# Optimization experiments

Hardware: AMD Instinct MI355X
Metric: run time of the kernel (lower is better)

The kernel has to match this reference:

```python
import jax, jax.numpy as jnp
import numpy as np
from jax import lax

B, C, H, W = 2, 64, 384, 384
WS = 8; NH = 4; HD = C // NH; S = WS * WS  # 64 tokens per window
EPS = 1e-5


def setup_inputs() -> dict:
    key = jax.random.key(0)
    ks = jax.random.split(key, 16)
    def n(k, shape, s=0.02):
        return jax.random.normal(k, shape, jnp.float32) * s
    return {
        "x": jax.random.normal(ks[0], (B, C, H, W), jnp.float32),
        "norm1_w": jnp.ones((C,), jnp.float32), "norm1_b": jnp.zeros((C,), jnp.float32),
        "qkv_w": n(ks[1], (3 * C, C)), "qkv_b": jnp.zeros((3 * C,), jnp.float32),
        "pos_bias": n(ks[2], (1, S, NH, NH), 0.01),  # faithful: bias over (tokens, heads, heads)
        "out_w": n(ks[3], (C, C)), "out_b": jnp.zeros((C,), jnp.float32),
        "convp_w": n(ks[4], (C, C)), "convp_b": jnp.zeros((C,), jnp.float32),
        "pw1_w": n(ks[5], (C, C, 1)), "pw1_b": jnp.zeros((C,), jnp.float32),
        "dw1_w": n(ks[6], (C, 1, 3)), "dw1_b": jnp.zeros((C,), jnp.float32),
        "tok_w": n(ks[7], (C, C)), "tok_b": jnp.zeros((C,), jnp.float32),
        "norm2_w": jnp.ones((C,), jnp.float32), "norm2_b": jnp.zeros((C,), jnp.float32),
        "leff_pw_w": n(ks[8], (C, C, 1, 1)),
        "leff_dw_w": n(ks[9], (C, 1, 3, 3)), "leff_dw_b": jnp.zeros((C,), jnp.float32),
        "fc1_w": n(ks[10], (4 * C, C)), "fc1_b": jnp.zeros((4 * C,), jnp.float32),
        "fc2_w": n(ks[11], (C, 4 * C)), "fc2_b": jnp.zeros((C,), jnp.float32),
    }


def _ln_c(x, w, b):
    # channel-wise LayerNorm (Restormer 'WithBias') on (B,C,H,W), biased variance
    mu = x.mean(axis=1, keepdims=True)
    var = ((x - mu) ** 2).mean(axis=1, keepdims=True)
    return (x - mu) / jnp.sqrt(var + EPS) * w[None, :, None, None] + b[None, :, None, None]


def _lin(x, w, b):
    return x @ w.T + b


def _win_part(x):
    # (B,C,H,W) -> (B*nw, S, C); H,W divisible by WS so pad is a no-op
    b = x.shape[0]
    x = x.reshape(b, C, H // WS, WS, W // WS, WS)
    return x.transpose(0, 2, 4, 3, 5, 1).reshape(-1, S, C)


def _win_merge(wins):
    b = wins.shape[0] // ((H // WS) * (W // WS))
    x = wins.reshape(b, H // WS, W // WS, WS, WS, C)
    return x.transpose(0, 5, 1, 3, 2, 4).reshape(b, C, H, W)


def _remsa(xw, qkv_w, qkv_b, pos_bias, out_w, out_b, convp_w, convp_b,
           pw1_w, pw1_b, dw1_w, dw1_b, tok_w, tok_b):
    bw = xw.shape[0]
    qkv = _lin(xw, qkv_w, qkv_b).reshape(bw, S, NH, 3 * HD)
    q, k, v = jnp.split(qkv, 3, axis=-1)  # each (bw, S, NH, HD)
    # Faithful to source: NO head transpose -> attention mixes across the heads axis
    scores = jnp.einsum('bshd,bsgd->bshg', q, k) * (HD ** -0.5) + pos_bias  # (bw,S,NH,NH)
    attn = jax.nn.softmax(scores, axis=-1)
    ao = jnp.einsum('bshg,bsgd->bshd', attn, v).reshape(bw, S, C)
    ao = _lin(ao, out_w, out_b)
    # convolutional branch
    xc = _lin(xw, convp_w, convp_b).transpose(0, 2, 1)  # (bw, C, S)
    xc = jnp.einsum('bcs,oc->bos', xc, pw1_w[:, :, 0]) + pw1_b[None, :, None]  # 1x1 conv1d
    xc = lax.conv_general_dilated(xc, dw1_w, (1,), 'SAME', feature_group_count=C,
                                  dimension_numbers=('NCH', 'OIH', 'NCH')) + dw1_b[None, :, None]
    xc = _lin(xc.transpose(0, 2, 1), tok_w, tok_b)
    return ao + xc


def _leff(x, pw_w, dw_w, dw_b, fc1_w, fc1_b, fc2_w, fc2_b):
    b = x.shape[0]
    y = lax.conv_general_dilated(x, pw_w, (1, 1), 'SAME',
                                 dimension_numbers=('NCHW', 'OIHW', 'NCHW'))  # 1x1, no bias
    y = lax.conv_general_dilated(y, dw_w, (1, 1), 'SAME', feature_group_count=C,
                                 dimension_numbers=('NCHW', 'OIHW', 'NCHW')) + dw_b[None, :, None, None]
    y = y.transpose(0, 2, 3, 1).reshape(b, H * W, C)
    y = jax.nn.gelu(_lin(y, fc1_w, fc1_b), approximate=False)
    y = _lin(y, fc2_w, fc2_b)
    return y.reshape(b, H, W, C).transpose(0, 3, 1, 2)


def reference(x, norm1_w, norm1_b, qkv_w, qkv_b, pos_bias, out_w, out_b,
              convp_w, convp_b, pw1_w, pw1_b, dw1_w, dw1_b, tok_w, tok_b,
              norm2_w, norm2_b, leff_pw_w, leff_dw_w, leff_dw_b,
              fc1_w, fc1_b, fc2_w, fc2_b):
    xw = _win_part(_ln_c(x, norm1_w, norm1_b))
    r = _win_merge(_remsa(xw, qkv_w, qkv_b, pos_bias, out_w, out_b, convp_w, convp_b,
                          pw1_w, pw1_b, dw1_w, dw1_b, tok_w, tok_b))
    x = x + r
    x = x + _leff(_ln_c(x, norm2_w, norm2_b), leff_pw_w, leff_dw_w, leff_dw_b,
                  fc1_w, fc1_b, fc2_w, fc2_b)
    return x
```

## Files before the change

### kernel.cpp

```cpp
#include <hip/hip_runtime.h>
#include <hip/hip_bf16.h>
#include <math.h>

#define Bn 2
#define Cc 64
#define Hh 384
#define Ww 384
#define HW (Hh*Ww)
#define Tt (Bn*HW)

using f32x4  = __attribute__((ext_vector_type(4))) float;
using bf16x8 = __attribute__((ext_vector_type(8))) short;


__device__ __forceinline__ unsigned short f2bf_u(float f) {
  return __builtin_bit_cast(unsigned short, __float2bfloat16(f));
}
__device__ __forceinline__ float bf2f(unsigned short u) {
  union { unsigned u; float f; } v; v.u = ((unsigned)u) << 16;
  return v.f;
}
__device__ __forceinline__ float gelu_exact(float v) {
  return 0.5f * v * (1.0f + erff(v * 0.70710678118654752f));
}

__device__ __forceinline__ void stage_wtile512(char* dst, const float* __restrict__ g, int rs, int tid) {
  const int row = tid >> 3, ks = tid & 7;
  const float* gp = g + (long)row * rs + ks * 8;
  float4 a = *(const float4*)gp;
  float4 b = *(const float4*)(gp + 4);
  bf16x8 o;
  o[0] = (short)f2bf_u(a.x); o[1] = (short)f2bf_u(a.y);
  o[2] = (short)f2bf_u(a.z); o[3] = (short)f2bf_u(a.w);
  o[4] = (short)f2bf_u(b.x); o[5] = (short)f2bf_u(b.y);
  o[6] = (short)f2bf_u(b.z); o[7] = (short)f2bf_u(b.w);
  *(bf16x8*)(dst + row * 128 + ((ks * 16) ^ ((row & 7) << 4))) = o;
}


__global__ __launch_bounds__(512, 4) void kA(
    const float* __restrict__ x, unsigned short* __restrict__ x1g, unsigned short* __restrict__ yg,
    const float* __restrict__ n1w, const float* __restrict__ n1b,
    const float* __restrict__ qkvw, const float* __restrict__ qkvb,
    const float* __restrict__ posb,
    const float* __restrict__ outw, const float* __restrict__ outb,
    const float* __restrict__ cpw, const float* __restrict__ cpb,
    const float* __restrict__ pw1w, const float* __restrict__ pw1b,
    const float* __restrict__ dw1w, const float* __restrict__ dw1b,
    const float* __restrict__ tokw, const float* __restrict__ tokb,
    const float* __restrict__ n2w, const float* __restrict__ n2b,
    const float* __restrict__ lpw) {
  __shared__ char sX[16384];
  __shared__ char sW0[8192];
  __shared__ char sW1[8192];
  __shared__ char sQ[49152];

  const int tid = threadIdx.x;
  const int lane = tid & 63, wid = tid >> 6;
  const int fr = lane & 15, kq = lane >> 4;
  const int rtok = wid * 16 + fr;
  const int c0own = kq * 16;
  const int iy = wid, ix = fr;
  const int blk = blockIdx.x;
  const int b = blk / 1152;
  const int rr = blk - b * 1152;
  const int wy = rr / 24, wxp = rr - (rr / 24) * 24;
  const int h0 = wy * 8, w0 = wxp * 16;
  const long ibase = (long)b * HW;

  float4 wr0, wr1;
  const int wrow = tid >> 3, wc0 = (tid & 7) * 8;
  auto WLOAD = [&](const float* g) {
    const float* p = g + (long)wrow * 64 + wc0;
    wr0 = *(const float4*)p; wr1 = *(const float4*)(p + 4);
  };
  auto WSTORE = [&](char* dst) {
    bf16x8 o;
    o[0]=(short)f2bf_u(wr0.x); o[1]=(short)f2bf_u(wr0.y); o[2]=(short)f2bf_u(wr0.z); o[3]=(short)f2bf_u(wr0.w);
    o[4]=(short)f2bf_u(wr1.x); o[5]=(short)f2bf_u(wr1.y); o[6]=(short)f2bf_u(wr1.z); o[7]=(short)f2bf_u(wr1.w);
    *(bf16x8*)(dst + wrow * 128 + ((2 * wc0) ^ ((wrow & 7) << 4))) = o;
  };

  WLOAD(cpw);
  const float* xb = x + ((long)(b * 64 + c0own)) * HW + (long)(h0 + iy) * Ww + (w0 + ix);
  float vx[16]; float s0 = 0.f, s1 = 0.f;
#pragma unroll
  for (int k = 0; k < 16; ++k) {
    float v = xb[(long)k * HW];
    vx[k] = v; s0 += v; s1 += v * v;
  }
  s0 += __shfl_xor(s0, 16); s0 += __shfl_xor(s0, 32);
  s1 += __shfl_xor(s1, 16); s1 += __shfl_xor(s1, 32);
  {
    float m = s0 * (1.f / 64.f);
    float ri = rsqrtf(s1 * (1.f / 64.f) - m * m + 1e-5f);
    const int swz = (rtok & 7) << 4;
#pragma unroll
    for (int q8 = 0; q8 < 2; ++q8) {
      bf16x8 o;
#pragma unroll
      for (int j = 0; j < 8; ++j) {
        int c = c0own + q8 * 8 + j;
        o[j] = (short)f2bf_u((vx[q8 * 8 + j] - m) * ri * n1w[c] + n1b[c]);
      }
      *(bf16x8*)(sX + rtok * 128 + ((c0own * 2 + q8 * 16) ^ swz)) = o;
    }
  }
  WSTORE(sW0); WLOAD(pw1w);
  __syncthreads();

  f32x4 acc[4], res[4];
  auto ZERO = [&](f32x4 a[4]) {
#pragma unroll
    for (int nt = 0; nt < 4; ++nt) a[nt] = (f32x4){0.f, 0.f, 0.f, 0.f};
  };
  auto GEMM = [&](const char* A, const char* W, f32x4 a[4]) {
#pragma unroll
    for (int kh = 0; kh < 2; ++kh) {
      const int arow = wid * 16 + fr;
      bf16x8 af = *(const bf16x8*)(A + arow * 128 + ((kh * 64 + kq * 16) ^ ((arow & 7) << 4)));
#pragma unroll
      for (int nt = 0; nt < 4; ++nt) {
        const int brow = nt * 16 + fr;
        bf16x8 bv = *(const bf16x8*)(W + brow * 128 + ((kh * 64 + kq * 16) ^ ((brow & 7) << 4)));
        a[nt] = __builtin_amdgcn_mfma_f32_16x16x32_bf16(af, bv, a[nt], 0, 0, 0);
      }
    }
  };
  auto EPI = [&](char* dst, f32x4 a[4], const float* bias) {
    const int rb = wid * 16 + kq * 4;
#pragma unroll
    for (int nt = 0; nt < 4; ++nt) {
      const int col = nt * 16 + fr;
      const float bv = bias[col];
#pragma unroll
      for (int reg = 0; reg < 4; ++reg) {
        const int row = rb + reg;
        *(unsigned short*)(dst + row * 128 + ((2 * col) ^ ((row & 7) << 4))) = f2bf_u(a[nt][reg] + bv);
      }
    }
  };
  char* t0 = sQ; char* t1 = sQ + 16384; char* t2 = sQ + 32768;
  float* sQf = (float*)sQ;

  ZERO(acc); GEMM(sX, sW0, acc); EPI(t0, acc, cpb);
  WSTORE(sW1); WLOAD(tokw);
  __syncthreads();
  ZERO(acc); GEMM(t0, sW1, acc); EPI(t1, acc, pw1b);
  WSTORE(sW0); WLOAD(qkvw);
  __syncthreads();
  {
    const int c = tid & 63, tq = tid >> 6;
    const int wl = tq >> 2, chunk = tq & 3;
    float wv0 = dw1w[c * 3], wv1 = dw1w[c * 3 + 1], wv2 = dw1w[c * 3 + 2], bia = dw1b[c];
#pragma unroll
    for (int k = 0; k < 16; ++k) {
      int s = chunk * 16 + k;
      int r0 = ((s >> 3) << 4) + wl * 8 + (s & 7);
      float v = bia + bf2f(*(const unsigned short*)(t1 + r0 * 128 + ((2 * c) ^ ((r0 & 7) << 4)))) * wv1;
      if (s > 0) {
        int rm = (((s - 1) >> 3) << 4) + wl * 8 + ((s - 1) & 7);
        v += bf2f(*(const unsigned short*)(t1 + rm * 128 + ((2 * c) ^ ((rm & 7) << 4)))) * wv0;
      }
      if (s < 63) {
        int rp = (((s + 1) >> 3) << 4) + wl * 8 + ((s + 1) & 7);
        v += bf2f(*(const unsigned short*)(t1 + rp * 128 + ((2 * c) ^ ((rp & 7) << 4)))) * wv2;
      }
      *(unsigned short*)(t0 + r0 * 128 + ((2 * c) ^ ((r0 & 7) << 4))) = f2bf_u(v);
    }
  }
  WSTORE(sW1); WLOAD(qkvw + 4096);
  __syncthreads();
  ZERO(res); GEMM(t0, sW0, res);
  __syncthreads();
  ZERO(acc); GEMM(sX, sW1, acc); EPI(t0, acc, qkvb);
  WSTORE(sW0); WLOAD(qkvw + 8192);
  __syncthreads();
  ZERO(acc); GEMM(sX, sW0, acc); EPI(t1, acc, qkvb + 64);
  WSTORE(sW1); WLOAD(outw);
  __syncthreads();
  ZERO(acc); GEMM(sX, sW1, acc); EPI(t2, acc, qkvb + 128);
  WSTORE(sW0); WLOAD(lpw);
  __syncthreads();
  {
    const int r = rtok;
    const int h = kq;
    const int s = ((r >> 4) << 3) + (r & 7);
    const int swz = (r & 7) << 4;
    auto LD16 = [&](int gcol, float* o) {
      const char* base = sQ + ((gcol >> 6) * 16384) + r * 128;
      int c0 = (gcol & 63) * 2;
      bf16x8 u = *(const bf16x8*)(base + (c0 ^ swz));
      bf16x8 w2_ = *(const bf16x8*)(base + ((c0 + 16) ^ swz));
#pragma unroll
      for (int j = 0; j < 8; ++j) {
        o[j] = bf2f((unsigned short)u[j]); o[8 + j] = bf2f((unsigned short)w2_[j]);
      }
    };
    float q0[16];
    LD16(48 * h, q0);
    float sc[4];
#pragma unroll
    for (int g = 0; g < 4; ++g) {
      float kk[16]; LD16(48 * g + 16, kk);
      float a = 0.f;
#pragma unroll
      for (int d = 0; d < 16; ++d) a += q0[d] * kk[d];
      sc[g] = a * 0.25f + posb[s * 16 + h * 4 + g];
    }
    float m = fmaxf(fmaxf(sc[0], sc[1]), fmaxf(sc[2], sc[3]));
    float e[4]; float tsum = 0.f;
#pragma unroll
    for (int g = 0; g < 4; ++g) { e[g] = __expf(sc[g] - m); tsum += e[g]; }
    float inv = 1.f / tsum;
    float ao[16];
#pragma unroll
    for (int d = 0; d < 16; ++d) ao[d] = 0.f;
#pragma unroll
    for (int g = 0; g < 4; ++g) {
      float vv[16]; LD16(48 * g + 32, vv);
#pragma unroll
      for (int d = 0; d < 16; ++d) ao[d] += e[g] * vv[d];
    }
    bf16x8 o1, o2;
#pragma unroll
    for (int j = 0; j < 8; ++j) { o1[j] = (short)f2bf_u(ao[j] * inv); o2[j] = (short)f2bf_u(ao[8 + j] * inv); }
    *(bf16x8*)(sX + r * 128 + ((h * 32) ^ swz)) = o1;
    *(bf16x8*)(sX + r * 128 + ((h * 32 + 16) ^ swz)) = o2;
  }
  WSTORE(sW1);
  __syncthreads();
  GEMM(sX, sW0, res);
  {
    const int rb = wid * 16 + kq * 4;
#pragma unroll
    for (int nt = 0; nt < 4; ++nt) {
      const int col = nt * 16 + fr;
      const float ob = outb[col] + tokb[col];
#pragma unroll
      for (int reg = 0; reg < 4; ++reg)
        sQf[(rb + reg) * 67 + col] = res[nt][reg] + ob;
    }
  }
  __syncthreads();
  {
    float ss0 = 0.f, ss1 = 0.f;
#pragma unroll
    for (int k = 0; k < 16; ++k) {
      float v = sQf[rtok * 67 + c0own + k] + vx[k];
      vx[k] = v; ss0 += v; ss1 += v * v;
    }
    ss0 += __shfl_xor(ss0, 16); ss0 += __shfl_xor(ss0, 32);
    ss1 += __shfl_xor(ss1, 16); ss1 += __shfl_xor(ss1, 32);
    float m = ss0 * (1.f / 64.f);
    float ri = rsqrtf(ss1 * (1.f / 64.f) - m * m + 1e-5f);
    const int swz = (rtok & 7) << 4;
    long t = ibase + (long)(h0 + iy) * Ww + (w0 + ix);
#pragma unroll
    for (int q8 = 0; q8 < 2; ++q8) {
      bf16x8 xo, no;
#pragma unroll
      for (int j = 0; j < 8; ++j) {
        int c = c0own + q8 * 8 + j;
        float v = vx[q8 * 8 + j];
        xo[j] = (short)f2bf_u(v);
        no[j] = (short)f2bf_u((v - m) * ri * n2w[c] + n2b[c]);
      }
      *(bf16x8*)((char*)x1g + t * 128 + (c0own + q8 * 8) * 2) = xo;
      *(bf16x8*)(sX + rtok * 128 + ((c0own * 2 + q8 * 16) ^ swz)) = no;
    }
  }
  __syncthreads();
  ZERO(acc); GEMM(sX, sW1, acc);
  {
    const int rb = wid * 16 + kq * 4;
#pragma unroll
    for (int nt = 0; nt < 4; ++nt) {
      const int col = nt * 16 + fr;
#pragma unroll
      for (int reg = 0; reg < 4; ++reg)
        sQf[(rb + reg) * 67 + col] = acc[nt][reg];
    }
  }
  __syncthreads();
  {
    long t = ibase + (long)(h0 + iy) * Ww + (w0 + ix);
#pragma unroll
    for (int q8 = 0; q8 < 2; ++q8) {
      bf16x8 o;
#pragma unroll
      for (int j = 0; j < 8; ++j)
        o[j] = (short)f2bf_u(sQf[rtok * 67 + c0own + q8 * 8 + j]);
      *(bf16x8*)((char*)yg + t * 128 + (c0own + q8 * 8) * 2) = o;
    }
  }
}


__global__ __launch_bounds__(512, 2) void kB(
    const unsigned short* __restrict__ yg, const unsigned short* __restrict__ x1g,
    float* __restrict__ out,
    const float* __restrict__ ldw, const float* __restrict__ ldb,
    const float* __restrict__ f1w, const float* __restrict__ f1b,
    const float* __restrict__ f2w, const float* __restrict__ f2b) {
  __shared__ char sZ0[8192];
  __shared__ char sZ1[8192];
  __shared__ char U[33792];
  __shared__ float wtab[640];

  const int tid = threadIdx.x;
  const int lane = tid & 63, wid = tid >> 6;
  const int fr = lane & 15, kq = lane >> 4;
  const int t_own = wid >> 2;
  const int wv = wid & 3;
  const int bid = blockIdx.x;
  const int b = bid / 1152;
  const int r2 = bid - b * 1152;
  const int hp = r2 / 6, wseg = r2 - (r2 / 6) * 6;
  const int h0 = hp * 2, w0 = wseg * 64;
  const long ibase = (long)b * HW;
  const int cbase = fr;
  const int rbase = wv * 16 + kq * 4;

  unsigned short x1r[4][4];
  {
    const long p0t = ibase + (long)(h0 + t_own) * Ww + w0;
#pragma unroll
    for (int nt = 0; nt < 4; ++nt) {
      int col = nt * 16 + cbase;
#pragma unroll
      for (int reg = 0; reg < 4; ++reg)
        x1r[nt][reg] = x1g[(p0t + rbase + reg) * 64 + col];
    }
  }

#pragma unroll
  for (int it = 0; it < 2; ++it) {
    int idx = it * 512 + tid;
    if (idx < 576) wtab[idx] = ldw[(idx & 63) * 9 + (idx >> 6)];
    else if (idx < 640) wtab[idx] = ldb[idx - 576];
  }

  for (int it = 0; it < 5; ++it) {
    int idx = it * 512 + tid;
    if (idx >= 2112) break;
    int hr = idx / 528;
    int rq = idx - hr * 528;
    int px = rq >> 3, c8 = rq & 7;
    int h = h0 - 1 + hr, w = w0 - 1 + px;
    uint4 v = make_uint4(0, 0, 0, 0);
    if (h >= 0 && h < Hh && w >= 0 && w < Ww) {
      long t = ibase + (long)h * Ww + w;
      v = *(const uint4*)((const char*)yg + t * 128 + c8 * 16);
    }
    int X = hr * 66 + px;
    *(uint4*)(U + X * 128 + ((c8 * 16) ^ ((X & 7) << 4))) = v;
  }
  __syncthreads();

  {
    const int c8l = tid & 7;
    const int c0 = c8l * 8;
#pragma unroll
    for (int it = 0; it < 2; ++it) {
      int task = it * 512 + tid;
      int r = task >> 9;
      int px = (task >> 3) & 63;
      float a8[8];
#pragma unroll
      for (int j = 0; j < 8; ++j) a8[j] = wtab[576 + c0 + j];
#pragma unroll
      for (int dy = 0; dy < 3; ++dy)
#pragma unroll
        for (int dx = 0; dx < 3; ++dx) {
          int X = (r + dy) * 66 + px + dx;
          bf16x8 v = *(const bf16x8*)(U + X * 128 + ((c8l * 16) ^ ((X & 7) << 4)));
          const float* wk = wtab + (dy * 3 + dx) * 64 + c0;
#pragma unroll
          for (int j = 0; j < 8; ++j) a8[j] += bf2f((unsigned short)v[j]) * wk[j];
        }
      char* sZ = r ? sZ1 : sZ0;
      bf16x8 o;
#pragma unroll
      for (int j = 0; j < 8; ++j) o[j] = (short)f2bf_u(a8[j]);
      *(bf16x8*)(sZ + px * 128 + ((c8l * 16) ^ ((px & 7) << 4))) = o;
    }
  }
  __syncthreads();

  char* sW  = U;
  char* sH0 = U + 8192;
  char* sH1 = U + 16384;
  char* sZt = t_own ? sZ1 : sZ0;
  char* sHt = t_own ? sH1 : sH0;
  f32x4 res[4];
#pragma unroll
  for (int nt = 0; nt < 4; ++nt) res[nt] = (f32x4){0.f, 0.f, 0.f, 0.f};

  for (int jc = 0; jc < 4; ++jc) {
    stage_wtile512(sW, f1w + jc * 4096, 64, tid);
    __syncthreads();
    {
      f32x4 acc[4];
#pragma unroll
      for (int nt = 0; nt < 4; ++nt) acc[nt] = (f32x4){0.f, 0.f, 0.f, 0.f};
#pragma unroll
      for (int kh = 0; kh < 2; ++kh) {
        const int arow = wv * 16 + fr;
        bf16x8 af = *(const bf16x8*)(sZt + arow * 128 + ((kh * 64 + kq * 16) ^ ((arow & 7) << 4)));
#pragma unroll
        for (int nt = 0; nt < 4; ++nt) {
          const int brow = nt * 16 + fr;
          bf16x8 bv = *(const bf16x8*)(sW + brow * 128 + ((kh * 64 + kq * 16) ^ ((brow & 7) << 4)));
          acc[nt] = __builtin_amdgcn_mfma_f32_16x16x32_bf16(af, bv, acc[nt], 0, 0, 0);
        }
      }
#pragma unroll
      for (int nt = 0; nt < 4; ++nt) {
        const int col = nt * 16 + cbase;
        const float bv = f1b[jc * 64 + col];
#pragma unroll
        for (int reg = 0; reg < 4; ++reg) {
          const int row = rbase + reg;
          *(unsigned short*)(sHt + row * 128 + ((col * 2) ^ ((row & 7) << 4))) =
              f2bf_u(gelu_exact(acc[nt][reg] + bv));
        }
      }
    }
    __syncthreads();
    stage_wtile512(sW, f2w + jc * 64, 256, tid);
    __syncthreads();
#pragma unroll
    for (int kh = 0; kh < 2; ++kh) {
      const int arow = wv * 16 + fr;
      bf16x8 af = *(const bf16x8*)(sHt + arow * 128 + ((kh * 64 + kq * 16) ^ ((arow & 7) << 4)));
#pragma unroll
      for (int nt = 0; nt < 4; ++nt) {
        const int brow = nt * 16 + fr;
        bf16x8 bv = *(const bf16x8*)(sW + brow * 128 + ((kh * 64 + kq * 16) ^ ((brow & 7) << 4)));
        res[nt] = __builtin_amdgcn_mfma_f32_16x16x32_bf16(af, bv, res[nt], 0, 0, 0);
      }
    }
    __syncthreads();
  }

  float* sO = (float*)U;
#pragma unroll
  for (int nt = 0; nt < 4; ++nt) {
    const int col = nt * 16 + cbase;
    const float bv = f2b[col];
#pragma unroll
    for (int reg = 0; reg < 4; ++reg) {
      const int row = rbase + reg;
      sO[t_own * 4160 + row * 65 + col] = res[nt][reg] + bv + bf2f(x1r[nt][reg]);
    }
  }
  __syncthreads();
  {
    const int t = tid >> 8;
    const int tt = tid & 255;
#pragma unroll
    for (int it = 0; it < 16; ++it) {
      int c = it * 4 + (tt >> 6);
      int wo = tt & 63;
      out[(((long)(b * Cc + c)) * Hh + (h0 + t)) * Ww + w0 + wo] = sO[t * 4160 + wo * 65 + c];
    }
  }
}


extern "C" void kernel_launch(void* const* d_in, const int* in_sizes, int n_in,
                              void* d_out, int out_size, void* d_ws, size_t ws_size,
                              hipStream_t stream) {
  const float* x    = (const float*)d_in[0];
  const float* n1w  = (const float*)d_in[1];
  const float* n1b  = (const float*)d_in[2];
  const float* qkvw = (const float*)d_in[3];
  const float* qkvb = (const float*)d_in[4];
  const float* posb = (const float*)d_in[5];
  const float* outw = (const float*)d_in[6];
  const float* outb = (const float*)d_in[7];
  const float* cpw  = (const float*)d_in[8];
  const float* cpb  = (const float*)d_in[9];
  const float* pw1w = (const float*)d_in[10];
  const float* pw1b = (const float*)d_in[11];
  const float* dw1w = (const float*)d_in[12];
  const float* dw1b = (const float*)d_in[13];
  const float* tokw = (const float*)d_in[14];
  const float* tokb = (const float*)d_in[15];
  const float* n2w  = (const float*)d_in[16];
  const float* n2b  = (const float*)d_in[17];
  const float* lpw  = (const float*)d_in[18];
  const float* ldw  = (const float*)d_in[19];
  const float* ldb  = (const float*)d_in[20];
  const float* f1w  = (const float*)d_in[21];
  const float* f1b  = (const float*)d_in[22];
  const float* f2w  = (const float*)d_in[23];
  const float* f2b  = (const float*)d_in[24];
  float* out = (float*)d_out;

  unsigned short* x1 = (unsigned short*)d_ws;
  unsigned short* y  = x1 + (size_t)Tt * 64;

  kA<<<dim3(2304), dim3(512), 0, stream>>>(x, x1, y, n1w, n1b, qkvw, qkvb, posb,
                                           outw, outb, cpw, cpb, pw1w, pw1b,
                                           dw1w, dw1b, tokw, tokb, n2w, n2b, lpw);
  kB<<<dim3(2304), dim3(512), 0, stream>>>(y, x1, out, ldw, ldb, f1w, f1b, f2w, f2b);
}
```

Before: 174.9 us.

## Double-buffer MLP weight tiles with register prefetch to overlap global loads

New measurement: 166.2 us. 5.0% less time.

```diff
diff --git a/kernel.cpp b/kernel.cpp
--- a/kernel.cpp
+++ b/kernel.cpp
@@ -22,19 +22,6 @@
 }
 __device__ __forceinline__ float gelu_exact(float v) {
   return 0.5f * v * (1.0f + erff(v * 0.70710678118654752f));
-}
-
-__device__ __forceinline__ void stage_wtile512(char* dst, const float* __restrict__ g, int rs, int tid) {
-  const int row = tid >> 3, ks = tid & 7;
-  const float* gp = g + (long)row * rs + ks * 8;
-  float4 a = *(const float4*)gp;
-  float4 b = *(const float4*)(gp + 4);
-  bf16x8 o;
-  o[0] = (short)f2bf_u(a.x); o[1] = (short)f2bf_u(a.y);
-  o[2] = (short)f2bf_u(a.z); o[3] = (short)f2bf_u(a.w);
-  o[4] = (short)f2bf_u(b.x); o[5] = (short)f2bf_u(b.y);
-  o[6] = (short)f2bf_u(b.z); o[7] = (short)f2bf_u(b.w);
-  *(bf16x8*)(dst + row * 128 + ((ks * 16) ^ ((row & 7) << 4))) = o;
 }
 
 
@@ -322,6 +309,19 @@
   const int cbase = fr;
   const int rbase = wv * 16 + kq * 4;
 
+  float4 wr0, wr1;
+  const int wrow = tid >> 3, wc0 = (tid & 7) * 8;
+  auto WLOAD = [&](const float* g, int rs) {
+    const float* p = g + (long)wrow * rs + wc0;
+    wr0 = *(const float4*)p; wr1 = *(const float4*)(p + 4);
+  };
+  auto WSTORE = [&](char* dst) {
+    bf16x8 o;
+    o[0]=(short)f2bf_u(wr0.x); o[1]=(short)f2bf_u(wr0.y); o[2]=(short)f2bf_u(wr0.z); o[3]=(short)f2bf_u(wr0.w);
+    o[4]=(short)f2bf_u(wr1.x); o[5]=(short)f2bf_u(wr1.y); o[6]=(short)f2bf_u(wr1.z); o[7]=(short)f2bf_u(wr1.w);
+    *(bf16x8*)(dst + wrow * 128 + ((2 * wc0) ^ ((wrow & 7) << 4))) = o;
+  };
+
   unsigned short x1r[4][4];
   {
     const long p0t = ibase + (long)(h0 + t_own) * Ww + w0;
@@ -356,6 +356,7 @@
     int X = hr * 66 + px;
     *(uint4*)(U + X * 128 + ((c8 * 16) ^ ((X & 7) << 4))) = v;
   }
+  WLOAD(f1w, 64);
   __syncthreads();
 
   {
@@ -388,18 +389,21 @@
   }
   __syncthreads();
 
-  char* sW  = U;
+  char* sWa = U;
   char* sH0 = U + 8192;
   char* sH1 = U + 16384;
+  char* sWb = U + 24576;
   char* sZt = t_own ? sZ1 : sZ0;
   char* sHt = t_own ? sH1 : sH0;
   f32x4 res[4];
 #pragma unroll
   for (int nt = 0; nt < 4; ++nt) res[nt] = (f32x4){0.f, 0.f, 0.f, 0.f};
 
+  WSTORE(sWa);
+  WLOAD(f2w, 256);
+  __syncthreads();
+
   for (int jc = 0; jc < 4; ++jc) {
-    stage_wtile512(sW, f1w + jc * 4096, 64, tid);
-    __syncthreads();
     {
       f32x4 acc[4];
 #pragma unroll
@@ -411,10 +415,12 @@
 #pragma unroll
         for (int nt = 0; nt < 4; ++nt) {
           const int brow = nt * 16 + fr;
-          bf16x8 bv = *(const bf16x8*)(sW + brow * 128 + ((kh * 64 + kq * 16) ^ ((brow & 7) << 4)));
+          bf16x8 bv = *(const bf16x8*)(sWa + brow * 128 + ((kh * 64 + kq * 16) ^ ((brow & 7) << 4)));
           acc[nt] = __builtin_amdgcn_mfma_f32_16x16x32_bf16(af, bv, acc[nt], 0, 0, 0);
         }
       }
+      WSTORE(sWb);
+      if (jc < 3) WLOAD(f1w + (jc + 1) * 4096, 64);
 #pragma unroll
       for (int nt = 0; nt < 4; ++nt) {
         const int col = nt * 16 + cbase;
@@ -428,8 +434,6 @@
       }
     }
     __syncthreads();
-    stage_wtile512(sW, f2w + jc * 64, 256, tid);
-    __syncthreads();
 #pragma unroll
     for (int kh = 0; kh < 2; ++kh) {
       const int arow = wv * 16 + fr;
@@ -437,10 +441,11 @@
 #pragma unroll
       for (int nt = 0; nt < 4; ++nt) {
         const int brow = nt * 16 + fr;
-        bf16x8 bv = *(const bf16x8*)(sW + brow * 128 + ((kh * 64 + kq * 16) ^ ((brow & 7) << 4)));
+        bf16x8 bv = *(const bf16x8*)(sWb + brow * 128 + ((kh * 64 + kq * 16) ^ ((brow & 7) << 4)));
         res[nt] = __builtin_amdgcn_mfma_f32_16x16x32_bf16(af, bv, res[nt], 0, 0, 0);
       }
     }
+    if (jc < 3) { WSTORE(sWa); WLOAD(f2w + (jc + 1) * 64, 256); }
     __syncthreads();
   }
 
```
